# Optimization experiments

Measured on AMD Instinct MI355X. Metric: run time of the kernel, lower is better.

The kernel has to match this reference:

```python
import jax, jax.numpy as jnp
import numpy as np

H, D, BLK, R = 12, 64, 64, 3  # heads, size_per_head, block size, rand blocks
NEG = -1e9


def setup_inputs() -> dict:
    key = jax.random.key(0)
    ks = jax.random.split(key, 6)
    B, S, W = 2, 4096, H * D
    M = S // BLK
    return {
        "from_tensor": jax.random.normal(ks[0], (B, S, W), jnp.float32),
        "to_tensor": jax.random.normal(ks[1], (B, S, W), jnp.float32),
        "Wq": jax.random.normal(ks[2], (W, H * D), jnp.float32) * 0.02,
        "bq": jnp.zeros((H * D,), jnp.float32),
        "Wk": jax.random.normal(ks[3], (W, H * D), jnp.float32) * 0.02,
        "bk": jnp.zeros((H * D,), jnp.float32),
        "Wv": jax.random.normal(ks[4], (W, H * D), jnp.float32) * 0.02,
        "bv": jnp.zeros((H * D,), jnp.float32),
        "to_mask": jnp.ones((B, S), jnp.int32),
        "rand_attn": jax.random.randint(ks[5], (H, M - 2, R), 0, M - 2, jnp.int32),
    }


def _bigbird_block_sparse(from_tensor, to_tensor, Wq, bq, Wk, bk, Wv, bv, to_mask, rand_attn):
    B, S, _ = from_tensor.shape
    M = S // BLK
    scale = 1.0 / np.sqrt(D).astype(np.float32)

    # QKV projections -> [B,H,S,D]
    q = (from_tensor @ Wq + bq).reshape(B, S, H, D).transpose(0, 2, 1, 3)
    k = (to_tensor @ Wk + bk).reshape(B, S, H, D).transpose(0, 2, 1, 3)
    v = (to_tensor @ Wv + bv).reshape(B, S, H, D).transpose(0, 2, 1, 3)

    bq_ = q.reshape(B, H, M, BLK, D)
    bk_ = k.reshape(B, H, M, BLK, D)
    bv_ = v.reshape(B, H, M, BLK, D)

    tm = to_mask.astype(q.dtype)          # [B,S]
    bm = tm.reshape(B, M, BLK)            # [B,M,BLK]

    # gather random key/value blocks per head: [B,H,M-2,R*BLK,D]
    ha = jnp.arange(H)[:, None, None]
    gk = bk_[:, ha, rand_attn].reshape(B, H, M - 2, R * BLK, D)
    gv = bv_[:, ha, rand_attn].reshape(B, H, M - 2, R * BLK, D)
    gm = bm[:, rand_attn].reshape(B, H, M - 2, R * BLK)

    def full_row(qblk):  # first/last query blocks attend to everything
        s = jnp.einsum('bhqd,bhkd->bhqk', qblk, k) * scale + (1 - tm)[:, None, None, :] * NEG
        return jnp.einsum('bhqk,bhkd->bhqd', jax.nn.softmax(s, -1), v)

    def sparse_row(qblk, k_cat, v_cat, m_cat):  # [B,H,BLK,D] x [B,H,L,D]
        s = jnp.einsum('bhqd,bhkd->bhqk', qblk, k_cat) * scale + (1 - m_cat)[:, :, None, :] * NEG
        return jnp.einsum('bhqk,bhkd->bhqd', jax.nn.softmax(s, -1), v_cat)

    c_first = full_row(bq_[:, :, 0])
    c_last = full_row(bq_[:, :, M - 1])

    # second row: blocks [0,1,2,last] + rand
    k2 = jnp.concatenate([bk_[:, :, 0], bk_[:, :, 1], bk_[:, :, 2], bk_[:, :, M - 1], gk[:, :, 0]], axis=2)
    v2 = jnp.concatenate([bv_[:, :, 0], bv_[:, :, 1], bv_[:, :, 2], bv_[:, :, M - 1], gv[:, :, 0]], axis=2)
    m2s = jnp.concatenate([bm[:, 0], bm[:, 1], bm[:, 2], bm[:, M - 1]], axis=-1)
    m2 = jnp.concatenate([jnp.broadcast_to(m2s[:, None], (B, H, 4 * BLK)), gm[:, :, 0]], axis=-1)
    c_second = sparse_row(bq_[:, :, 1], k2, v2, m2)

    # second-to-last row: blocks [0,M-3,M-2,M-1] + rand
    k3 = jnp.concatenate([bk_[:, :, 0], bk_[:, :, M - 3], bk_[:, :, M - 2], bk_[:, :, M - 1], gk[:, :, M - 3]], axis=2)
    v3 = jnp.concatenate([bv_[:, :, 0], bv_[:, :, M - 3], bv_[:, :, M - 2], bv_[:, :, M - 1], gv[:, :, M - 3]], axis=2)
    m3s = jnp.concatenate([bm[:, 0], bm[:, M - 3], bm[:, M - 2], bm[:, M - 1]], axis=-1)
    m3 = jnp.concatenate([jnp.broadcast_to(m3s[:, None], (B, H, 4 * BLK)), gm[:, :, M - 3]], axis=-1)
    c_secondlast = sparse_row(bq_[:, :, M - 2], k3, v3, m3)

    # middle rows 2..M-3: band(prev,self,next) + rand + global first/last blocks
    L = M - 4
    band_k = jnp.concatenate([bk_[:, :, 1:M - 3], bk_[:, :, 2:M - 2], bk_[:, :, 3:M - 1]], axis=3)  # [B,H,L,3BLK,D]
    band_v = jnp.concatenate([bv_[:, :, 1:M - 3], bv_[:, :, 2:M - 2], bv_[:, :, 3:M - 1]], axis=3)
    band_m = jnp.concatenate([bm[:, 1:M - 3], bm[:, 2:M - 2], bm[:, 3:M - 1]], axis=-1)  # [B,L,3BLK]

    k_mid = jnp.concatenate([
        band_k, gk[:, :, 1:M - 3],
        jnp.broadcast_to(bk_[:, :, 0:1], (B, H, L, BLK, D)),
        jnp.broadcast_to(bk_[:, :, M - 1:M], (B, H, L, BLK, D))], axis=3)
    v_mid = jnp.concatenate([
        band_v, gv[:, :, 1:M - 3],
        jnp.broadcast_to(bv_[:, :, 0:1], (B, H, L, BLK, D)),
        jnp.broadcast_to(bv_[:, :, M - 1:M], (B, H, L, BLK, D))], axis=3)
    m_mid = jnp.concatenate([
        jnp.broadcast_to(band_m[:, None], (B, H, L, 3 * BLK)),
        gm[:, :, 1:M - 3],
        jnp.broadcast_to(bm[:, None, None, 0], (B, H, L, BLK)),
        jnp.broadcast_to(bm[:, None, None, M - 1], (B, H, L, BLK))], axis=-1)

    s_mid = jnp.einsum('bhlqd,bhlkd->bhlqk', bq_[:, :, 2:M - 2], k_mid) * scale
    s_mid = s_mid + (1 - m_mid)[:, :, :, None, :] * NEG
    c_mid = jnp.einsum('bhlqk,bhlkd->bhlqd', jax.nn.softmax(s_mid, -1), v_mid)

    ctx = jnp.concatenate([
        c_first[:, :, None], c_second[:, :, None], c_mid,
        c_secondlast[:, :, None], c_last[:, :, None]], axis=2)  # [B,H,M,BLK,D]
    return ctx.reshape(B, H, S, D).transpose(0, 2, 1, 3)  # [B,S,H,D]


def reference(from_tensor, to_tensor, Wq, bq, Wk, bk, Wv, bv, to_mask, rand_attn):
    return _bigbird_block_sparse(from_tensor, to_tensor, Wq, bq, Wk, bk, Wv, bv, to_mask, rand_attn)
```

## Files before the change

### kernel.cpp

```cpp
#include <hip/hip_runtime.h>

typedef __attribute__((ext_vector_type(4))) float f32x4;
typedef __attribute__((ext_vector_type(8))) __bf16 bf16x8;
typedef __attribute__((ext_vector_type(8))) unsigned short u16x8;
typedef __attribute__((ext_vector_type(4))) unsigned short u16x4;
typedef __attribute__((ext_vector_type(2))) unsigned int u32x2;

#define LOG2E 1.4426950408889634f

__device__ __forceinline__ unsigned short f2bf(float f) {
  unsigned u = __builtin_bit_cast(unsigned, f);
  u += 0x7fffu + ((u >> 16) & 1u);
  return (unsigned short)(u >> 16);
}

__device__ __forceinline__ unsigned cvtpk(float lo, float hi) {
  unsigned r;
  asm("v_cvt_pk_bf16_f32 %0, %1, %2" : "=v"(r) : "v"(lo), "v"(hi));
  return r;
}

__device__ __forceinline__ f32x4 mfma16(bf16x8 a, bf16x8 b, f32x4 c) {
  return __builtin_amdgcn_mfma_f32_16x16x32_bf16(a, b, c, 0, 0, 0);
}

__device__ __forceinline__ void gload_lds16(const void* g, void* l) {
  __builtin_amdgcn_global_load_lds(
      (const __attribute__((address_space(1))) void*)g,
      (__attribute__((address_space(3))) void*)l, 16, 0, 0);
}

#define NQK 6291456
#define NX 6291456
#define NW 589824

__global__ __launch_bounds__(256) void prep_kernel(
    const float* __restrict__ Wq, const float* __restrict__ Wk,
    const float* __restrict__ Wv, const float* __restrict__ from_t,
    const float* __restrict__ to_t, unsigned short* __restrict__ Wt,
    unsigned short* __restrict__ xb) {
  __shared__ float tile[64][65];
  const int bid = blockIdx.x;
  const int t = threadIdx.x;
  if (bid < 432) {
    const int z = bid / 144, rest = bid % 144;
    const float* __restrict__ src = (z == 0) ? Wq : (z == 1) ? Wk : Wv;
    unsigned short* __restrict__ dst = Wt + (size_t)z * NW;
    const int k0 = (rest / 12) * 64, n0 = (rest % 12) * 64;
    const int r = t >> 4, c4 = (t & 15) * 4;
#pragma unroll
    for (int p = 0; p < 4; ++p) {
      int rr = r + p * 16;
      f32x4 v = *(const f32x4*)(src + (size_t)(k0 + rr) * 768 + n0 + c4);
#pragma unroll
      for (int j = 0; j < 4; ++j) tile[rr][c4 + j] = v[j];
    }
    __syncthreads();
#pragma unroll
    for (int p = 0; p < 4; ++p) {
      int rn = r + p * 16;
      u16x4 o;
#pragma unroll
      for (int j = 0; j < 4; ++j) o[j] = f2bf(tile[c4 + j][rn]);
      *(u16x4*)(dst + (size_t)(n0 + rn) * 768 + k0 + c4) = o;
    }
  } else {
    const int idx = bid - 432;
    const int y = idx / 3072, xi = idx % 3072;
    const float* __restrict__ src = y ? to_t : from_t;
    unsigned short* __restrict__ dst = xb + (size_t)y * NX;
    const size_t i = ((size_t)xi * 256 + t) * 8;
    f32x4 a = *(const f32x4*)(src + i);
    f32x4 b = *(const f32x4*)(src + i + 4);
    u16x8 o;
#pragma unroll
    for (int j = 0; j < 4; ++j) { o[j] = f2bf(a[j]); o[j + 4] = f2bf(b[j]); }
    *(u16x8*)(dst + i) = o;
  }
}

__global__ __launch_bounds__(256) void qkv_gemm_kernel(
    const unsigned short* __restrict__ Xb, const unsigned short* __restrict__ Wt,
    const float* __restrict__ bq, const float* __restrict__ bk,
    const float* __restrict__ bv, unsigned short* __restrict__ qkvQK,
    unsigned short* __restrict__ vt, int zoff, int cpx) {
  __shared__ unsigned short A_lds[2][8192];
  __shared__ unsigned short B_lds[2][8192];
  const int bid0 = blockIdx.x;
  const int bid = (bid0 & 7) * cpx + (bid0 >> 3);
  const int z = zoff + bid / 384;
  const int rem = bid % 384;
  const int bm = rem / 6, bn = rem % 6;
  const unsigned short* __restrict__ X = Xb + (z ? (size_t)NX : 0);
  const unsigned short* __restrict__ Wz = Wt + (size_t)z * NW;
  const float* __restrict__ bias = (z == 0) ? bq : (z == 1) ? bk : bv;
  const int t = threadIdx.x, lane = t & 63, w = t >> 6;
  const int wm = (w >> 1) * 64, wn = (w & 1) * 64;
  const int l15 = lane & 15, cc = lane >> 4;

  f32x4 acc[4][4];
#pragma unroll
  for (int i = 0; i < 4; ++i)
#pragma unroll
    for (int j = 0; j < 4; ++j) acc[i][j] = (f32x4){0.f, 0.f, 0.f, 0.f};

  const unsigned short* Abase = X + (size_t)bm * 128 * 768;
  const unsigned short* Bbase = Wz + (size_t)bn * 128 * 768;

  auto STAGE = [&](int ks, int bufi) {
#pragma unroll
    for (int p = 0; p < 4; ++p) {
      int wb = p * 4 + w;
      int ch = wb * 64 + lane;
      int r = ch >> 3, sl = ch & 7;
      int g = sl ^ (r & 7);
      gload_lds16(Abase + (size_t)r * 768 + ks * 64 + g * 8,
                  &A_lds[bufi][wb * 512]);
      gload_lds16(Bbase + (size_t)r * 768 + ks * 64 + g * 8,
                  &B_lds[bufi][wb * 512]);
    }
  };

  STAGE(0, 0);

  for (int ks = 0; ks < 12; ++ks) {
    const int cur = ks & 1;
    if (ks < 11) {
      STAGE(ks + 1, cur ^ 1);
      asm volatile("s_waitcnt vmcnt(8)" ::: "memory");
    } else {
      asm volatile("s_waitcnt vmcnt(0)" ::: "memory");
    }
    __builtin_amdgcn_s_barrier();
    __builtin_amdgcn_sched_barrier(0);

    bf16x8 af[4][2], bfr[4][2];
#pragma unroll
    for (int mi = 0; mi < 4; ++mi) {
      int row = wm + mi * 16 + l15;
      const char* rp = (const char*)A_lds[cur] + row * 128;
#pragma unroll
      for (int kk = 0; kk < 2; ++kk)
        af[mi][kk] = *(const bf16x8*)(rp + (((cc + 4 * kk) ^ (row & 7)) << 4));
    }
#pragma unroll
    for (int ni = 0; ni < 4; ++ni) {
      int row = wn + ni * 16 + l15;
      const char* rp = (const char*)B_lds[cur] + row * 128;
#pragma unroll
      for (int kk = 0; kk < 2; ++kk)
        bfr[ni][kk] = *(const bf16x8*)(rp + (((cc + 4 * kk) ^ (row & 7)) << 4));
    }
#pragma unroll
    for (int kk = 0; kk < 2; ++kk)
#pragma unroll
      for (int mi = 0; mi < 4; ++mi)
#pragma unroll
        for (int ni = 0; ni < 4; ++ni)
          acc[mi][ni] = mfma16(af[mi][kk], bfr[ni][kk], acc[mi][ni]);
    asm volatile("s_waitcnt lgkmcnt(0)" ::: "memory");
    __builtin_amdgcn_s_barrier();
  }

  if (z < 2) {
    const float qscale = (z == 0) ? 0.125f * LOG2E : 1.0f;
    unsigned short* __restrict__ dst = qkvQK + (size_t)z * NQK;
#pragma unroll
    for (int ni = 0; ni < 4; ++ni) {
      int gn = bn * 128 + wn + ni * 16 + l15;
      float bv_ = bias[gn];
      int hh = gn >> 6, dd = gn & 63;
#pragma unroll
      for (int mi = 0; mi < 4; ++mi) {
#pragma unroll
        for (int r = 0; r < 4; ++r) {
          int gm = bm * 128 + wm + mi * 16 + cc * 4 + r;
          int bb = gm >> 12, s = gm & 4095;
          float val = (acc[mi][ni][r] + bv_) * qscale;
          dst[((((size_t)bb * 12 + hh) * 4096 + s) * 64) + dd] = f2bf(val);
        }
      }
    }
  } else {
#pragma unroll
    for (int ni = 0; ni < 4; ++ni) {
      int gn = bn * 128 + wn + ni * 16 + l15;
      float bv_ = bias[gn];
      int hh = gn >> 6, dd = gn & 63;
#pragma unroll
      for (int mi = 0; mi < 4; ++mi) {
        int gm0 = bm * 128 + wm + mi * 16 + cc * 4;
        int bb = gm0 >> 12, s0 = gm0 & 4095;
        u16x4 o;
#pragma unroll
        for (int r = 0; r < 4; ++r) o[r] = f2bf(acc[mi][ni][r] + bv_);
        *(u16x4*)(vt + ((size_t)(bb * 12 + hh) * 64 + dd) * 4096 + s0) = o;
      }
    }
  }
}

__global__ __launch_bounds__(256) void attn_kernel(
    const unsigned short* __restrict__ qkvQK, const unsigned short* __restrict__ vt,
    const int* __restrict__ to_mask, const int* __restrict__ rand_attn,
    float* __restrict__ out, float* __restrict__ part_o,
    float* __restrict__ part_ml) {
  __shared__ unsigned short K_lds[2][4096];
  __shared__ unsigned short VT_lds[2][4096];
  __shared__ unsigned short P_lds[4][1024];
  __shared__ float penal[8][64];
  __shared__ int blist[8];

  const int bid0 = blockIdx.x;
  const int bid = (bid0 & 7) * 234 + (bid0 >> 3);
  const int bh = bid / 78, r78 = bid % 78;
  const int h = bh % 12, b = bh / 12;
  const int t = threadIdx.x, lane = t & 63, w = t >> 6;
  const int l15 = lane & 15, cc = lane >> 4;

  int m, nblk, chunk = 0;
  bool full;
  if (r78 < 62) {
    full = false;
    m = r78 + 1;
    nblk = (m == 1 || m == 62) ? 7 : 8;
    if (t == 0) {
      const int* rp = rand_attn + ((size_t)h * 62 + (m - 1)) * 3;
      if (m == 1) {
        blist[0] = 0; blist[1] = 1; blist[2] = 2; blist[3] = 63;
        blist[4] = rp[0]; blist[5] = rp[1]; blist[6] = rp[2];
      } else if (m == 62) {
        blist[0] = 0; blist[1] = 61; blist[2] = 62; blist[3] = 63;
        blist[4] = rp[0]; blist[5] = rp[1]; blist[6] = rp[2];
      } else {
        blist[0] = m - 1; blist[1] = m; blist[2] = m + 1;
        blist[3] = rp[0]; blist[4] = rp[1]; blist[5] = rp[2];
        blist[6] = 0; blist[7] = 63;
      }
    }
  } else {
    full = true;
    int fr = r78 - 62;
    chunk = fr & 7;
    m = (fr >> 3) ? 63 : 0;
    nblk = 8;
    if (t < 8) blist[t] = chunk * 8 + t;
  }

  const unsigned short* qp = qkvQK + (((size_t)b * 12 + h) * 4096 + m * 64) * 64;
  const unsigned short* kp = qkvQK + NQK + (((size_t)b * 12 + h) * 4096) * 64;
  const unsigned short* vtp = vt + (((size_t)b * 12 + h) * 64) * 4096;

  int loff[2];
  const unsigned short *kpl[2], *vpl[2];
#pragma unroll
  for (int p = 0; p < 2; ++p) {
    int wb = p * 4 + w;
    int ch = wb * 64 + lane;
    int rr = ch >> 3;
    int g = (ch & 7) ^ (rr & 7);
    loff[p] = wb * 512;
    kpl[p] = kp + rr * 64 + g * 8;
    vpl[p] = vtp + rr * 4096 + g * 8;
  }

  bf16x8 aq[2];
  {
    int qrow = w * 16 + l15;
    aq[0] = *(const bf16x8*)(qp + qrow * 64 + cc * 8);
    aq[1] = *(const bf16x8*)(qp + qrow * 64 + 32 + cc * 8);
  }

  float m_run = -INFINITY, l_run = 0.f;
  f32x4 o_acc[4];
#pragma unroll
  for (int dg = 0; dg < 4; ++dg) o_acc[dg] = (f32x4){0.f, 0.f, 0.f, 0.f};

  char* pw = (char*)P_lds[w];
  const int swz = (l15 & 7) << 4;

  auto STAGE_K = [&](int kb, int bufi) {
    const size_t ko = (size_t)kb * 4096;
    gload_lds16(kpl[0] + ko, &K_lds[bufi][loff[0]]);
    gload_lds16(kpl[1] + ko, &K_lds[bufi][loff[1]]);
  };
  auto STAGE_V = [&](int kb, int bufi) {
    const size_t vo = (size_t)kb * 64;
    gload_lds16(vpl[0] + vo, &VT_lds[bufi][loff[0]]);
    gload_lds16(vpl[1] + vo, &VT_lds[bufi][loff[1]]);
  };

  auto QK = [&](int bufi, int slot, float s[4][4]) {
    const char* kbase = (const char*)K_lds[bufi];
    __builtin_amdgcn_s_setprio(1);
#pragma unroll
    for (int kg = 0; kg < 4; ++kg) {
      int krow = kg * 16 + l15;
      const char* rp = kbase + krow * 128;
      int sz = (krow & 7) << 4;
      bf16x8 k0 = *(const bf16x8*)(rp + ((cc << 4) ^ sz));
      bf16x8 k1 = *(const bf16x8*)(rp + (((cc + 4) << 4) ^ sz));
      f32x4 zz = (f32x4){0.f, 0.f, 0.f, 0.f};
      zz = mfma16(k0, aq[0], zz);
      zz = mfma16(k1, aq[1], zz);
      f32x4 pen = *(const f32x4*)(&penal[slot][kg * 16 + cc * 4]);
#pragma unroll
      for (int r = 0; r < 4; ++r) s[kg][r] = zz[r] + pen[r];
    }
    __builtin_amdgcn_s_setprio(0);
  };

  __syncthreads();

  {
    int ib = w;
#pragma unroll
    for (int pp = 0; pp < 2; ++pp, ib += 4)
      if (ib < nblk)
        penal[ib][lane] =
            (1.0f - (float)to_mask[(size_t)b * 4096 + blist[ib] * 64 + lane]) *
            (-1e9f * LOG2E);
  }
  STAGE_K(blist[0], 0);
  STAGE_V(blist[0], 0);
  STAGE_K(blist[1], 1);
  asm volatile("s_waitcnt vmcnt(4) lgkmcnt(0)" ::: "memory");
  __builtin_amdgcn_s_barrier();
  __builtin_amdgcn_sched_barrier(0);

  float sm[4][4];
  QK(0, 0, sm);

  for (int ib = 0; ib < nblk; ++ib) {
    asm volatile("s_waitcnt vmcnt(0)" ::: "memory");
    __builtin_amdgcn_s_barrier();
    __builtin_amdgcn_sched_barrier(0);

    if (ib + 2 < nblk) STAGE_K(blist[ib + 2], ib & 1);
    if (ib + 1 < nblk) STAGE_V(blist[ib + 1], (ib + 1) & 1);

    float sn[4][4];
    if (ib + 1 < nblk) QK((ib + 1) & 1, ib + 1, sn);

    float mk[4];
#pragma unroll
    for (int kg = 0; kg < 4; ++kg)
      mk[kg] = fmaxf(fmaxf(sm[kg][0], sm[kg][1]), fmaxf(sm[kg][2], sm[kg][3]));
    float mx = fmaxf(fmaxf(mk[0], mk[1]), fmaxf(mk[2], mk[3]));
    mx = fmaxf(mx, __shfl_xor(mx, 16, 64));
    mx = fmaxf(mx, __shfl_xor(mx, 32, 64));

    if (!__all(mx - m_run <= 8.0f)) {
      float mn = fmaxf(m_run, mx);
      float fac = exp2f(m_run - mn);
      m_run = mn;
      l_run *= fac;
      float fr_[4];
#pragma unroll
      for (int r = 0; r < 4; ++r) fr_[r] = __shfl(fac, cc * 4 + r, 64);
#pragma unroll
      for (int dg = 0; dg < 4; ++dg)
#pragma unroll
        for (int r = 0; r < 4; ++r) o_acc[dg][r] *= fr_[r];
    }

    float rs = 0.f;
#pragma unroll
    for (int kg = 0; kg < 4; ++kg) {
      float p0 = exp2f(sm[kg][0] - m_run), p1 = exp2f(sm[kg][1] - m_run);
      float p2 = exp2f(sm[kg][2] - m_run), p3 = exp2f(sm[kg][3] - m_run);
      rs += (p0 + p1) + (p2 + p3);
      u32x2 wv;
      wv[0] = cvtpk(p0, p1);
      wv[1] = cvtpk(p2, p3);
      *(u32x2*)(pw + l15 * 128 + ((kg * 32 + cc * 8) ^ swz)) = wv;
    }
    rs += __shfl_xor(rs, 16, 64);
    rs += __shfl_xor(rs, 32, 64);
    l_run += rs;

    __builtin_amdgcn_wave_barrier();
    bf16x8 ap0 = *(const bf16x8*)(pw + l15 * 128 + ((cc << 4) ^ swz));
    bf16x8 ap1 = *(const bf16x8*)(pw + l15 * 128 + (((cc + 4) << 4) ^ swz));

    const char* vbase = (const char*)VT_lds[ib & 1];
    __builtin_amdgcn_s_setprio(1);
#pragma unroll
    for (int dg = 0; dg < 4; ++dg) {
      int drow = dg * 16 + l15;
      const char* vb = vbase + drow * 128;
      int sz = (drow & 7) << 4;
      bf16x8 v0 = *(const bf16x8*)(vb + ((cc << 4) ^ sz));
      bf16x8 v1 = *(const bf16x8*)(vb + (((cc + 4) << 4) ^ sz));
      o_acc[dg] = mfma16(ap0, v0, o_acc[dg]);
      o_acc[dg] = mfma16(ap1, v1, o_acc[dg]);
    }
    __builtin_amdgcn_s_setprio(0);

    if (ib + 1 < nblk) {
#pragma unroll
      for (int kg = 0; kg < 4; ++kg)
#pragma unroll
        for (int r = 0; r < 4; ++r) sm[kg][r] = sn[kg][r];
    }
  }

  if (!full) {
    float inv[4];
#pragma unroll
    for (int r = 0; r < 4; ++r) inv[r] = 1.0f / __shfl(l_run, cc * 4 + r, 64);
#pragma unroll
    for (int r = 0; r < 4; ++r) {
      int s = m * 64 + w * 16 + cc * 4 + r;
#pragma unroll
      for (int dg = 0; dg < 4; ++dg) {
        int d = dg * 16 + l15;
        out[(((size_t)b * 4096 + s) * 12 + h) * 64 + d] = o_acc[dg][r] * inv[r];
      }
    }
  } else {
    const int row = (b * 12 + h) * 2 + (m ? 1 : 0);
    float* po = part_o + (((size_t)row * 8 + chunk) * 64) * 64;
    float* pml = part_ml + ((size_t)row * 8 + chunk) * 128;
#pragma unroll
    for (int r = 0; r < 4; ++r) {
      int q = w * 16 + cc * 4 + r;
#pragma unroll
      for (int dg = 0; dg < 4; ++dg) {
        int d = dg * 16 + l15;
        po[q * 64 + d] = o_acc[dg][r];
      }
    }
    if (cc == 0) {
      pml[w * 16 + l15] = m_run;
      pml[64 + w * 16 + l15] = l_run;
    }
  }
}

__global__ __launch_bounds__(256) void combine_kernel(
    const float* __restrict__ part_o, const float* __restrict__ part_ml,
    float* __restrict__ out) {
  const int row = blockIdx.x;
  const int b = row / 24, h = (row >> 1) % 12, m = (row & 1) ? 63 : 0;
  const int t = threadIdx.x;
  const int q = t >> 2, d0 = (t & 3) * 16;

  float mc[8], lc[8];
  float M = -INFINITY;
#pragma unroll
  for (int c = 0; c < 8; ++c) {
    const float* pml = part_ml + ((size_t)row * 8 + c) * 128;
    mc[c] = pml[q];
    lc[c] = pml[64 + q];
    M = fmaxf(M, mc[c]);
  }
  float wgt[8], L = 0.f;
#pragma unroll
  for (int c = 0; c < 8; ++c) {
    wgt[c] = exp2f(mc[c] - M);
    L += wgt[c] * lc[c];
  }
  f32x4 acc[4];
#pragma unroll
  for (int j = 0; j < 4; ++j) acc[j] = (f32x4){0.f, 0.f, 0.f, 0.f};
#pragma unroll
  for (int c = 0; c < 8; ++c) {
    const float* po = part_o + (((size_t)row * 8 + c) * 64 + q) * 64 + d0;
#pragma unroll
    for (int j = 0; j < 4; ++j) {
      f32x4 v = *(const f32x4*)(po + j * 4);
#pragma unroll
      for (int e = 0; e < 4; ++e) acc[j][e] += wgt[c] * v[e];
    }
  }
  const float inv = 1.0f / L;
  const int s = m * 64 + q;
  float* op = out + (((size_t)b * 4096 + s) * 12 + h) * 64 + d0;
#pragma unroll
  for (int j = 0; j < 4; ++j) {
    f32x4 v;
#pragma unroll
    for (int e = 0; e < 4; ++e) v[e] = acc[j][e] * inv;
    *(f32x4*)(op + j * 4) = v;
  }
}

extern "C" void kernel_launch(void* const* d_in, const int* in_sizes, int n_in,
                              void* d_out, int out_size, void* d_ws,
                              size_t ws_size, hipStream_t stream) {
  (void)in_sizes; (void)n_in; (void)out_size;
  const float* from_t = (const float*)d_in[0];
  const float* to_t = (const float*)d_in[1];
  const float* Wq = (const float*)d_in[2];
  const float* bq = (const float*)d_in[3];
  const float* Wk = (const float*)d_in[4];
  const float* bk = (const float*)d_in[5];
  const float* Wv = (const float*)d_in[6];
  const float* bv = (const float*)d_in[7];
  const int* to_mask = (const int*)d_in[8];
  const int* rand_attn = (const int*)d_in[9];
  float* out = (float*)d_out;

  unsigned short* Wt = (unsigned short*)d_ws;
  unsigned short* qkvQK = Wt + (size_t)3 * NW;
  unsigned short* Xb = qkvQK + (size_t)2 * NQK;

  const size_t part_elems = (size_t)48 * 8 * 64 * 64 + (size_t)48 * 8 * 128;
  const size_t fused_bytes =
      ((size_t)3 * NW + 2 * NQK + 2 * NX + NQK) * 2 + part_elems * 4;

  if (ws_size >= fused_bytes) {
    unsigned short* vt = Xb + (size_t)2 * NX;
    float* part_o = (float*)Xb;
    float* part_ml = part_o + (size_t)48 * 8 * 64 * 64;

    prep_kernel<<<dim3(6576), dim3(256), 0, stream>>>(Wq, Wk, Wv, from_t, to_t,
                                                      Wt, Xb);
    qkv_gemm_kernel<<<dim3(1152), dim3(256), 0, stream>>>(
        Xb, Wt, bq, bk, bv, qkvQK, vt, 0, 144);
    attn_kernel<<<dim3(1872), dim3(256), 0, stream>>>(
        qkvQK, vt, to_mask, rand_attn, out, part_o, part_ml);
    combine_kernel<<<dim3(48), dim3(256), 0, stream>>>(part_o, part_ml, out);
  } else {
    unsigned short* vt = Xb;
    float* part_o = (float*)(Xb + (size_t)NX);
    float* part_ml = part_o + (size_t)48 * 8 * 64 * 64;

    prep_kernel<<<dim3(6576), dim3(256), 0, stream>>>(Wq, Wk, Wv, from_t, to_t,
                                                      Wt, Xb);
    qkv_gemm_kernel<<<dim3(768), dim3(256), 0, stream>>>(
        Xb, Wt, bq, bk, bv, qkvQK, vt, 0, 96);
    qkv_gemm_kernel<<<dim3(384), dim3(256), 0, stream>>>(
        Xb, Wt, bq, bk, bv, qkvQK, vt, 2, 48);
    attn_kernel<<<dim3(1872), dim3(256), 0, stream>>>(
        qkvQK, vt, to_mask, rand_attn, out, part_o, part_ml);
    combine_kernel<<<dim3(48), dim3(256), 0, stream>>>(part_o, part_ml, out);
  }
}
```

Measured before the change: 109.6 us.

## Feed P to PV MFMA from registers by permuting V^T fragment loads

Drops the per-wave LDS round trip for the softmax probability tile. The packed bf16 P values stay in registers and go straight in as the MFMA A operand. To match that register layout, the V^T operand is gathered as four 8-byte LDS reads with XOR-swizzled addresses instead of two 16-byte reads. The P_lds buffer goes away, and launch bounds now request 4 blocks per CU. The cost is more, narrower LDS reads for V and tighter register limits.

```diff
diff --git a/kernel.cpp b/kernel.cpp
--- a/kernel.cpp
+++ b/kernel.cpp
@@ -4,7 +4,6 @@
 typedef __attribute__((ext_vector_type(8))) __bf16 bf16x8;
 typedef __attribute__((ext_vector_type(8))) unsigned short u16x8;
 typedef __attribute__((ext_vector_type(4))) unsigned short u16x4;
-typedef __attribute__((ext_vector_type(2))) unsigned int u32x2;
 
 #define LOG2E 1.4426950408889634f
 
@@ -200,14 +199,13 @@
   }
 }
 
-__global__ __launch_bounds__(256) void attn_kernel(
+__global__ __launch_bounds__(256, 4) void attn_kernel(
     const unsigned short* __restrict__ qkvQK, const unsigned short* __restrict__ vt,
     const int* __restrict__ to_mask, const int* __restrict__ rand_attn,
     float* __restrict__ out, float* __restrict__ part_o,
     float* __restrict__ part_ml) {
   __shared__ unsigned short K_lds[2][4096];
   __shared__ unsigned short VT_lds[2][4096];
-  __shared__ unsigned short P_lds[4][1024];
   __shared__ float penal[8][64];
   __shared__ int blist[8];
 
@@ -264,6 +262,13 @@
     vpl[p] = vtp + rr * 4096 + g * 8;
   }
 
+  int vaddr[4];
+#pragma unroll
+  for (int dg = 0; dg < 4; ++dg) {
+    int d = dg * 16 + l15;
+    vaddr[dg] = d * 128 + ((((cc >> 1) ^ (d & 7)) << 4)) + (cc & 1) * 8;
+  }
+
   bf16x8 aq[2];
   {
     int qrow = w * 16 + l15;
@@ -275,9 +280,6 @@
   f32x4 o_acc[4];
 #pragma unroll
   for (int dg = 0; dg < 4; ++dg) o_acc[dg] = (f32x4){0.f, 0.f, 0.f, 0.f};
-
-  char* pw = (char*)P_lds[w];
-  const int swz = (l15 & 7) << 4;
 
   auto STAGE_K = [&](int kb, int bufi) {
     const size_t ko = (size_t)kb * 4096;
@@ -331,6 +333,9 @@
   float sm[4][4];
   QK(0, 0, sm);
 
+  union PF { unsigned u[4]; bf16x8 v; };
+  union VF { u16x4 h2[2]; bf16x8 v; };
+
   for (int ib = 0; ib < nblk; ++ib) {
     asm volatile("s_waitcnt vmcnt(0)" ::: "memory");
     __builtin_amdgcn_s_barrier();
@@ -365,35 +370,35 @@
     }
 
     float rs = 0.f;
+    unsigned pk[8];
 #pragma unroll
     for (int kg = 0; kg < 4; ++kg) {
       float p0 = exp2f(sm[kg][0] - m_run), p1 = exp2f(sm[kg][1] - m_run);
       float p2 = exp2f(sm[kg][2] - m_run), p3 = exp2f(sm[kg][3] - m_run);
       rs += (p0 + p1) + (p2 + p3);
-      u32x2 wv;
-      wv[0] = cvtpk(p0, p1);
-      wv[1] = cvtpk(p2, p3);
-      *(u32x2*)(pw + l15 * 128 + ((kg * 32 + cc * 8) ^ swz)) = wv;
+      pk[kg * 2] = cvtpk(p0, p1);
+      pk[kg * 2 + 1] = cvtpk(p2, p3);
     }
     rs += __shfl_xor(rs, 16, 64);
     rs += __shfl_xor(rs, 32, 64);
     l_run += rs;
 
-    __builtin_amdgcn_wave_barrier();
-    bf16x8 ap0 = *(const bf16x8*)(pw + l15 * 128 + ((cc << 4) ^ swz));
-    bf16x8 ap1 = *(const bf16x8*)(pw + l15 * 128 + (((cc + 4) << 4) ^ swz));
-
-    const char* vbase = (const char*)VT_lds[ib & 1];
+    PF a0, a1;
+    a0.u[0] = pk[0]; a0.u[1] = pk[1]; a0.u[2] = pk[2]; a0.u[3] = pk[3];
+    a1.u[0] = pk[4]; a1.u[1] = pk[5]; a1.u[2] = pk[6]; a1.u[3] = pk[7];
+
+    const char* vbuf = (const char*)VT_lds[ib & 1];
     __builtin_amdgcn_s_setprio(1);
 #pragma unroll
     for (int dg = 0; dg < 4; ++dg) {
-      int drow = dg * 16 + l15;
-      const char* vb = vbase + drow * 128;
-      int sz = (drow & 7) << 4;
-      bf16x8 v0 = *(const bf16x8*)(vb + ((cc << 4) ^ sz));
-      bf16x8 v1 = *(const bf16x8*)(vb + (((cc + 4) << 4) ^ sz));
-      o_acc[dg] = mfma16(ap0, v0, o_acc[dg]);
-      o_acc[dg] = mfma16(ap1, v1, o_acc[dg]);
+      int a00 = vaddr[dg];
+      VF f0, f1;
+      f0.h2[0] = *(const u16x4*)(vbuf + a00);
+      f0.h2[1] = *(const u16x4*)(vbuf + (a00 ^ 32));
+      f1.h2[0] = *(const u16x4*)(vbuf + (a00 ^ 64));
+      f1.h2[1] = *(const u16x4*)(vbuf + (a00 ^ 96));
+      o_acc[dg] = mfma16(a0.v, f0.v, o_acc[dg]);
+      o_acc[dg] = mfma16(a1.v, f1.v, o_acc[dg]);
     }
     __builtin_amdgcn_s_setprio(0);
 
```

New measurement: 108.2 us. About the same (-1.3%).
